# Kernel optimization log

Measured on AMD Instinct MI355X. Metric: run time of the kernel, lower is better.

Reference implementation:

```python
import jax, jax.numpy as jnp
import numpy as np

N, D, K = 65536, 4096, 16
LN_EPS = 1e-5
SN_EPS = 1e-12
MIN_NORM = 1e-15


def setup_inputs() -> dict:
    key = jax.random.key(0)
    k1, k2, k3, k4 = jax.random.split(key, 4)
    return {
        "x": jax.random.normal(k1, (N, D), dtype=jnp.float32),
        "gamma": jnp.ones((D,), dtype=jnp.float32),
        "beta": jnp.zeros((D,), dtype=jnp.float32),
        "W": jax.random.normal(k2, (K, D), dtype=jnp.float32) * 0.02,
        "u": jax.random.normal(k3, (K,), dtype=jnp.float32),
        "log_scale": jnp.float32(-2.0),
    }


def _l2_normalize(v, eps=SN_EPS):
    return v / (jnp.linalg.norm(v) + eps)


def reference(x, gamma, beta, W, u, log_scale):
    # LayerNorm over last dim
    mean = jnp.mean(x, axis=-1, keepdims=True)
    var = jnp.mean(jnp.square(x - mean), axis=-1, keepdims=True)
    xn = (x - mean) * jax.lax.rsqrt(var + LN_EPS) * gamma + beta

    # spectral norm of W: one power iteration (torch spectral_norm forward)
    v = _l2_normalize(W.T @ u)           # [D]
    u_new = _l2_normalize(W @ v)         # [K]
    sigma = u_new @ (W @ v)              # scalar, top singular value estimate
    W_sn = W / sigma

    # linear (no bias) + learned scale
    vout = xn @ W_sn.T                   # [N, K]
    scale = jax.nn.sigmoid(log_scale) * 0.5
    vout = vout * scale

    # Poincare ball expmap0 with c=1: tanh(||v||) * v / ||v||
    vnorm = jnp.maximum(jnp.linalg.norm(vout, axis=-1, keepdims=True), MIN_NORM)
    return jnp.tanh(vnorm) * vout / vnorm
```

## Files before the change

### kernel.cpp

```cpp
#include <hip/hip_runtime.h>
#include <hip/hip_bf16.h>


#define ND 4096
#define NK 16
#define NROWS 65536

using f32x4  = __attribute__((ext_vector_type(4))) float;
using bf16x8 = __attribute__((ext_vector_type(8))) short;

#define GWB_OFF  0u
#define T_OFF    131072u
#define PART_OFF 147456u
#define SC_OFF   149568u

__device__ __forceinline__ unsigned short f2bf(float f) {
    union { __hip_bfloat16 h; unsigned short u; } cv;
    cv.h = __float2bfloat16(f);
    return cv.u;
}

__global__ __launch_bounds__(256) void prep_a(
    const float* __restrict__ W, const float* __restrict__ gamma,
    const float* __restrict__ beta, const float* __restrict__ u,
    float* __restrict__ ws_t, unsigned short* __restrict__ ws_gwb,
    float* __restrict__ ws_part)
{
    const int d = blockIdx.x * 256 + threadIdx.x;
    float uu[NK];
#pragma unroll
    for (int k = 0; k < NK; ++k) uu[k] = u[k];
    const float g = gamma[d], b = beta[d];
    float w[NK];
#pragma unroll
    for (int k = 0; k < NK; ++k) w[k] = W[k * ND + d];
    float t = 0.f;
#pragma unroll
    for (int k = 0; k < NK; ++k) t = fmaf(w[k], uu[k], t);
    ws_t[d] = t;
    const int c8 = d >> 3, j = d & 7;
#pragma unroll
    for (int k = 0; k < NK; ++k) ws_gwb[(c8 * NK + k) * 8 + j] = f2bf(g * w[k]);

    __shared__ float red[256][34];
    red[threadIdx.x][0] = t * t;
#pragma unroll
    for (int k = 0; k < NK; ++k) {
        red[threadIdx.x][1 + k]  = g * w[k];
        red[threadIdx.x][17 + k] = b * w[k];
    }
    __syncthreads();
    for (int off = 128; off > 0; off >>= 1) {
        if (threadIdx.x < off)
            for (int v = 0; v < 33; ++v)
                red[threadIdx.x][v] += red[threadIdx.x + off][v];
        __syncthreads();
    }
    if (threadIdx.x < 33) ws_part[blockIdx.x * 33 + threadIdx.x] = red[0][threadIdx.x];
}

__global__ __launch_bounds__(256) void prep_b(
    const float* __restrict__ W, const float* __restrict__ ws_t,
    const float* __restrict__ ws_part, const float* __restrict__ log_scale,
    float* __restrict__ sc)
{
    __shared__ float tot[33];
    __shared__ float red[256][17];
    const int tid = threadIdx.x;
    if (tid < 33) {
        float s = 0.f;
        for (int b = 0; b < 16; ++b) s += ws_part[b * 33 + tid];
        tot[tid] = s;
    }
    __syncthreads();
    const float inv_nt = 1.0f / (sqrtf(tot[0]) + 1e-12f);
    float sp[NK];
#pragma unroll
    for (int k = 0; k < NK; ++k) sp[k] = 0.f;
    for (int j = 0; j < 16; ++j) {
        const int d = tid * 16 + j;
        const float vd = ws_t[d] * inv_nt;
#pragma unroll
        for (int k = 0; k < NK; ++k) sp[k] = fmaf(W[k * ND + d], vd, sp[k]);
    }
#pragma unroll
    for (int k = 0; k < NK; ++k) red[tid][k] = sp[k];
    __syncthreads();
    for (int off = 128; off > 0; off >>= 1) {
        if (tid < off)
            for (int v = 0; v < NK; ++v) red[tid][v] += red[tid + off][v];
        __syncthreads();
    }
    if (tid == 0) {
        float ns2 = 0.f;
        for (int k = 0; k < NK; ++k) ns2 += red[0][k] * red[0][k];
        const float sigma = ns2 / (sqrtf(ns2) + 1e-12f);
        const float ls = log_scale[0];
        const float scale = 0.5f / (1.0f + expf(-ls));
        sc[0] = scale / sigma;
        for (int k = 0; k < NK; ++k) { sc[1 + k] = tot[1 + k]; sc[17 + k] = tot[17 + k]; }
    }
}

__global__ __launch_bounds__(1024, 4) void hyp_main(
    const float* __restrict__ x, const unsigned short* __restrict__ gwb_g,
    const float* __restrict__ sc, float* __restrict__ out)
{
    __shared__ unsigned short gwb[ND * NK];
    {
        const uint4* src = (const uint4*)gwb_g;
        uint4* dst = (uint4*)gwb;
#pragma unroll
        for (int i = 0; i < 8; ++i)
            dst[threadIdx.x + i * 1024] = src[threadIdx.x + i * 1024];
    }
    __syncthreads();

    const int lane = threadIdx.x & 63;
    const int wid  = threadIdx.x >> 6;
    const int tile = (blockIdx.x << 4) + wid;
    const int lr = lane & 15;
    const int lc = lane >> 4;

    const float* xp = x + (size_t)(tile * 16 + lr) * ND + lc * 8;
    const unsigned short* lp = gwb + lane * 8;

    f32x4 acc = {0.f, 0.f, 0.f, 0.f};
    float s1 = 0.f, s2 = 0.f;

#pragma unroll 4
    for (int c = 0; c < ND; c += 32) {
        f32x4 xa = *(const f32x4*)(xp + c);
        f32x4 xb = *(const f32x4*)(xp + c + 4);
        bf16x8 a;
        a[0] = (short)f2bf(xa[0]); a[1] = (short)f2bf(xa[1]);
        a[2] = (short)f2bf(xa[2]); a[3] = (short)f2bf(xa[3]);
        a[4] = (short)f2bf(xb[0]); a[5] = (short)f2bf(xb[1]);
        a[6] = (short)f2bf(xb[2]); a[7] = (short)f2bf(xb[3]);
        s1 += ((xa[0] + xa[1]) + (xa[2] + xa[3])) + ((xb[0] + xb[1]) + (xb[2] + xb[3]));
        s2 = fmaf(xa[0], xa[0], s2); s2 = fmaf(xa[1], xa[1], s2);
        s2 = fmaf(xa[2], xa[2], s2); s2 = fmaf(xa[3], xa[3], s2);
        s2 = fmaf(xb[0], xb[0], s2); s2 = fmaf(xb[1], xb[1], s2);
        s2 = fmaf(xb[2], xb[2], s2); s2 = fmaf(xb[3], xb[3], s2);
        bf16x8 b = *(const bf16x8*)(lp + c * 16);
        acc = __builtin_amdgcn_mfma_f32_16x16x32_bf16(a, b, acc, 0, 0, 0);
    }

    s1 += __shfl_xor(s1, 16); s1 += __shfl_xor(s1, 32);
    s2 += __shfl_xor(s2, 16); s2 += __shfl_xor(s2, 32);
    const float mean = s1 * (1.0f / ND);
    const float var  = s2 * (1.0f / ND) - mean * mean;
    const float rstd = rsqrtf(var + 1e-5f);

    const float coef = sc[0];
    const float gk = sc[1 + lr];
    const float bk = sc[17 + lr];

    float vout[4];
#pragma unroll
    for (int j = 0; j < 4; ++j) {
        const int r = lc * 4 + j;
        const float m_r  = __shfl(mean, r);
        const float rs_r = __shfl(rstd, r);
        vout[j] = coef * (fmaf(-m_r, gk, acc[j]) * rs_r + bk);
    }

    float nsq[4];
#pragma unroll
    for (int j = 0; j < 4; ++j) nsq[j] = vout[j] * vout[j];
#pragma unroll
    for (int m = 1; m < 16; m <<= 1) {
#pragma unroll
        for (int j = 0; j < 4; ++j) nsq[j] += __shfl_xor(nsq[j], m);
    }

#pragma unroll
    for (int j = 0; j < 4; ++j) {
        float nv = sqrtf(nsq[j]);
        nv = fmaxf(nv, 1e-15f);
        const float fac = tanhf(nv) / nv;
        out[(size_t)(tile * 16 + lc * 4 + j) * NK + lr] = vout[j] * fac;
    }
}

extern "C" void kernel_launch(void* const* d_in, const int* in_sizes, int n_in,
                              void* d_out, int out_size, void* d_ws, size_t ws_size,
                              hipStream_t stream) {
    const float* x     = (const float*)d_in[0];
    const float* gamma = (const float*)d_in[1];
    const float* beta  = (const float*)d_in[2];
    const float* W     = (const float*)d_in[3];
    const float* u     = (const float*)d_in[4];
    const float* ls    = (const float*)d_in[5];

    char* ws = (char*)d_ws;
    unsigned short* ws_gwb = (unsigned short*)(ws + GWB_OFF);
    float* ws_t    = (float*)(ws + T_OFF);
    float* ws_part = (float*)(ws + PART_OFF);
    float* sc      = (float*)(ws + SC_OFF);
    float* out     = (float*)d_out;

    prep_a<<<16, 256, 0, stream>>>(W, gamma, beta, u, ws_t, ws_gwb, ws_part);
    prep_b<<<1, 256, 0, stream>>>(W, ws_t, ws_part, ls, sc);
    hyp_main<<<256, 1024, 0, stream>>>(x, ws_gwb, sc, out);
}
```

Measured before the change: 208.6 us.

## Remap K-chunk permutation for coalesced x loads and software-prefetch next chunk

Changes the per-lane assignment of x columns within each 32-wide chunk: each lane now reads two 16-byte pieces 64 bytes apart instead of 32 contiguous bytes. The gamma*W bf16 table is permuted to match in prep_a, so the MFMA dot products stay consistent. The main loop loads the next chunk's x before processing the current one, and the first x loads are issued before the shared-memory fill and barrier so they overlap with it. The intent is better memory coalescing and hiding global-load latency in this bandwidth-bound kernel, at the cost of a few extra live registers.

```diff
diff --git a/kernel.cpp b/kernel.cpp
--- a/kernel.cpp
+++ b/kernel.cpp
@@ -38,9 +38,14 @@
 #pragma unroll
     for (int k = 0; k < NK; ++k) t = fmaf(w[k], uu[k], t);
     ws_t[d] = t;
-    const int c8 = d >> 3, j = d & 7;
-#pragma unroll
-    for (int k = 0; k < NK; ++k) ws_gwb[(c8 * NK + k) * 8 + j] = f2bf(g * w[k]);
+
+    const int s  = d >> 5;
+    const int wq = d & 31;
+    const int lc = (wq >> 2) & 3;
+    const int j  = (wq & 3) | ((wq >> 4) << 2);
+    const int base = s * 512 + lc * 128 + j;
+#pragma unroll
+    for (int k = 0; k < NK; ++k) ws_gwb[base + k * 8] = f2bf(g * w[k]);
 
     __shared__ float red[256][34];
     red[threadIdx.x][0] = t * t;
@@ -77,8 +82,8 @@
     float sp[NK];
 #pragma unroll
     for (int k = 0; k < NK; ++k) sp[k] = 0.f;
-    for (int j = 0; j < 16; ++j) {
-        const int d = tid * 16 + j;
+    for (int jj = 0; jj < 16; ++jj) {
+        const int d = tid * 16 + jj;
         const float vd = ws_t[d] * inv_nt;
 #pragma unroll
         for (int k = 0; k < NK; ++k) sp[k] = fmaf(W[k * ND + d], vd, sp[k]);
@@ -95,8 +100,7 @@
         float ns2 = 0.f;
         for (int k = 0; k < NK; ++k) ns2 += red[0][k] * red[0][k];
         const float sigma = ns2 / (sqrtf(ns2) + 1e-12f);
-        const float ls = log_scale[0];
-        const float scale = 0.5f / (1.0f + expf(-ls));
+        const float scale = 0.5f / (1.0f + expf(-log_scale[0]));
         sc[0] = scale / sigma;
         for (int k = 0; k < NK; ++k) { sc[1 + k] = tot[1 + k]; sc[17 + k] = tot[17 + k]; }
     }
@@ -107,14 +111,6 @@
     const float* __restrict__ sc, float* __restrict__ out)
 {
     __shared__ unsigned short gwb[ND * NK];
-    {
-        const uint4* src = (const uint4*)gwb_g;
-        uint4* dst = (uint4*)gwb;
-#pragma unroll
-        for (int i = 0; i < 8; ++i)
-            dst[threadIdx.x + i * 1024] = src[threadIdx.x + i * 1024];
-    }
-    __syncthreads();
 
     const int lane = threadIdx.x & 63;
     const int wid  = threadIdx.x >> 6;
@@ -122,39 +118,59 @@
     const int lr = lane & 15;
     const int lc = lane >> 4;
 
-    const float* xp = x + (size_t)(tile * 16 + lr) * ND + lc * 8;
+    const float* xp = x + (size_t)(tile * 16 + lr) * ND + lc * 4;
     const unsigned short* lp = gwb + lane * 8;
+
+    f32x4 xa = *(const f32x4*)(xp);
+    f32x4 xb = *(const f32x4*)(xp + 16);
+
+    {
+        const uint4* src = (const uint4*)gwb_g;
+        uint4* dst = (uint4*)gwb;
+#pragma unroll
+        for (int i = 0; i < 8; ++i)
+            dst[threadIdx.x + i * 1024] = src[threadIdx.x + i * 1024];
+    }
+    __syncthreads();
+
+    const float coef = sc[0];
+    const float gk = sc[1 + lr];
+    const float bk = sc[17 + lr];
 
     f32x4 acc = {0.f, 0.f, 0.f, 0.f};
     float s1 = 0.f, s2 = 0.f;
 
+#define PROCESS(XA, XB, SS) do {                                          \
+        bf16x8 afrag;                                                     \
+        afrag[0] = (short)f2bf(XA[0]); afrag[1] = (short)f2bf(XA[1]);     \
+        afrag[2] = (short)f2bf(XA[2]); afrag[3] = (short)f2bf(XA[3]);     \
+        afrag[4] = (short)f2bf(XB[0]); afrag[5] = (short)f2bf(XB[1]);     \
+        afrag[6] = (short)f2bf(XB[2]); afrag[7] = (short)f2bf(XB[3]);     \
+        s1 += ((XA[0] + XA[1]) + (XA[2] + XA[3]))                         \
+            + ((XB[0] + XB[1]) + (XB[2] + XB[3]));                        \
+        s2 = fmaf(XA[0], XA[0], s2); s2 = fmaf(XA[1], XA[1], s2);         \
+        s2 = fmaf(XA[2], XA[2], s2); s2 = fmaf(XA[3], XA[3], s2);         \
+        s2 = fmaf(XB[0], XB[0], s2); s2 = fmaf(XB[1], XB[1], s2);         \
+        s2 = fmaf(XB[2], XB[2], s2); s2 = fmaf(XB[3], XB[3], s2);         \
+        bf16x8 bfrag = *(const bf16x8*)(lp + (SS) * 512);                 \
+        acc = __builtin_amdgcn_mfma_f32_16x16x32_bf16(afrag, bfrag, acc, 0, 0, 0); \
+    } while (0)
+
 #pragma unroll 4
-    for (int c = 0; c < ND; c += 32) {
-        f32x4 xa = *(const f32x4*)(xp + c);
-        f32x4 xb = *(const f32x4*)(xp + c + 4);
-        bf16x8 a;
-        a[0] = (short)f2bf(xa[0]); a[1] = (short)f2bf(xa[1]);
-        a[2] = (short)f2bf(xa[2]); a[3] = (short)f2bf(xa[3]);
-        a[4] = (short)f2bf(xb[0]); a[5] = (short)f2bf(xb[1]);
-        a[6] = (short)f2bf(xb[2]); a[7] = (short)f2bf(xb[3]);
-        s1 += ((xa[0] + xa[1]) + (xa[2] + xa[3])) + ((xb[0] + xb[1]) + (xb[2] + xb[3]));
-        s2 = fmaf(xa[0], xa[0], s2); s2 = fmaf(xa[1], xa[1], s2);
-        s2 = fmaf(xa[2], xa[2], s2); s2 = fmaf(xa[3], xa[3], s2);
-        s2 = fmaf(xb[0], xb[0], s2); s2 = fmaf(xb[1], xb[1], s2);
-        s2 = fmaf(xb[2], xb[2], s2); s2 = fmaf(xb[3], xb[3], s2);
-        bf16x8 b = *(const bf16x8*)(lp + c * 16);
-        acc = __builtin_amdgcn_mfma_f32_16x16x32_bf16(a, b, acc, 0, 0, 0);
-    }
+    for (int s = 0; s < 127; ++s) {
+        f32x4 na = *(const f32x4*)(xp + (s + 1) * 32);
+        f32x4 nb = *(const f32x4*)(xp + (s + 1) * 32 + 16);
+        PROCESS(xa, xb, s);
+        xa = na; xb = nb;
+    }
+    PROCESS(xa, xb, 127);
+#undef PROCESS
 
     s1 += __shfl_xor(s1, 16); s1 += __shfl_xor(s1, 32);
     s2 += __shfl_xor(s2, 16); s2 += __shfl_xor(s2, 32);
     const float mean = s1 * (1.0f / ND);
     const float var  = s2 * (1.0f / ND) - mean * mean;
     const float rstd = rsqrtf(var + 1e-5f);
-
-    const float coef = sc[0];
-    const float gk = sc[1 + lr];
-    const float bk = sc[17 + lr];
 
     float vout[4];
 #pragma unroll
```

Result: slower. 214.7 us (+2.9%).
